# Performance work log

Hardware: AMD Instinct MI355X
Metric: run time of the kernel (lower is better)

## Reference

```python
import jax, jax.numpy as jnp
import numpy as np

PRESENCE_W = 1.0
L1_W = 1.0
B, N, M = 64, 2048, 64


def setup_inputs() -> dict:
    key = jax.random.key(0)
    k1, k2, k3, k4 = jax.random.split(key, 4)
    return {
        "predict_scores": jax.random.normal(k1, (B, N, 2), dtype=jnp.float32),
        "predict_boxes": jax.random.uniform(k2, (B, N, 4), dtype=jnp.float32),
        "scores": jax.random.randint(k3, (B, M), 0, 2, dtype=jnp.int32),
        "boxes": jax.random.uniform(k4, (B, M, 4), dtype=jnp.float32),
    }


def _cost(ps, pb, gs, gb):
    # presence[b,n,m] = -ps[b,n,gs[b,m]]
    b, n, _ = ps.shape
    m = gs.shape[1]
    idx = jnp.broadcast_to(gs[:, None, :].astype(jnp.int32), (b, n, m))
    presence = -jnp.take_along_axis(ps, idx, axis=2)            # (B,N,M)
    l1 = jnp.abs(pb[:, :, None, :] - gb[:, None, :, :]).sum(-1)  # (B,N,M)
    return PRESENCE_W * presence + L1_W * l1


def _hungarian(cost):
    # Jonker-Volgenant shortest-augmenting-path LSA (same optimum as
    # scipy.optimize.linear_sum_assignment). cost: (n, m) with n <= m.
    # Returns col4row: for each row i, the assigned column.
    n, m = cost.shape
    INF = np.inf
    u = np.zeros(n + 1)
    v = np.zeros(m + 1)
    p = np.zeros(m + 1, dtype=np.int64)   # col -> assigned row (1-based), 0=free
    way = np.zeros(m + 1, dtype=np.int64)
    for i in range(1, n + 1):
        p[0] = i
        j0 = 0
        minv = np.full(m + 1, INF)
        used = np.zeros(m + 1, dtype=bool)
        while True:
            used[j0] = True
            i0 = p[j0]
            free = ~used[1:]
            cur = cost[i0 - 1] - u[i0] - v[1:]
            mv = minv[1:]
            wy = way[1:]
            upd = free & (cur < mv)
            mv[upd] = cur[upd]
            wy[upd] = j0
            masked = np.where(free, mv, INF)
            j1 = int(np.argmin(masked)) + 1
            delta = masked[j1 - 1]
            used_idx = np.flatnonzero(used)
            u[p[used_idx]] += delta
            v[used_idx] -= delta
            mv[free] -= delta
            j0 = j1
            if p[j0] == 0:
                break
        while j0:
            j1 = way[j0]
            p[j0] = p[j1]
            j0 = j1
    col4row = np.zeros(n, dtype=np.int64)
    for j in range(1, m + 1):
        if p[j] > 0:
            col4row[p[j] - 1] = j - 1
    return col4row


def reference(predict_scores, predict_boxes, scores, boxes):
    cost = _cost(predict_scores, predict_boxes, scores, boxes)  # (B,N,M)
    c = np.asarray(jax.device_get(cost), dtype=np.float64)
    rows, cols = [], []
    for b in range(c.shape[0]):
        # transpose so the smaller side (M targets) is rows, like scipy does
        pred_for_gt = _hungarian(c[b].T)         # (M,) prediction index per target
        order = np.argsort(pred_for_gt)
        rows.append(pred_for_gt[order])          # sorted prediction indices
        cols.append(order.astype(np.int64))      # matching target indices
    row_ind = jnp.asarray(np.stack(rows), dtype=jnp.int32)  # (B,M)
    col_ind = jnp.asarray(np.stack(cols), dtype=jnp.int32)  # (B,M)
    return cost, row_ind, col_ind
```

## Files before the change

kernel.cpp:

```cpp
#include <hip/hip_runtime.h>
#include <math.h>
#include <limits.h>

#define Bb 64
#define Nn 2048
#define Mm 64

__device__ __forceinline__ float cost1(const float4 pb4, const float4 gb4,
                                       const float2 p2, const int g) {
    const float psv = (g == 0) ? p2.x : p2.y;
    float l1 = fabsf(pb4.x - gb4.x);
    l1 += fabsf(pb4.y - gb4.y);
    l1 += fabsf(pb4.z - gb4.z);
    l1 += fabsf(pb4.w - gb4.w);
    return (-psv) + l1;
}

__device__ __forceinline__ double readlane_f64_63(double x) {
    const long long v = __double_as_longlong(x);
    const int lo = __builtin_amdgcn_readlane((int)v, 63);
    const int hi = __builtin_amdgcn_readlane((int)(v >> 32), 63);
    return __longlong_as_double(((long long)hi << 32) | (unsigned int)lo);
}

__device__ __forceinline__ double readlane_f64(double x, int sl) {
    const long long v = __double_as_longlong(x);
    const int lo = __builtin_amdgcn_readlane((int)v, sl);
    const int hi = __builtin_amdgcn_readlane((int)(v >> 32), sl);
    return __longlong_as_double(((long long)hi << 32) | (unsigned int)lo);
}

__device__ __forceinline__ float readlane_f32(float x, int sl) {
    return __int_as_float(__builtin_amdgcn_readlane(__float_as_int(x), sl));
}

__device__ __forceinline__ void cost_tileA_t(
    int blk, int t, const float* __restrict__ ps, const float* __restrict__ pb,
    const int* __restrict__ gs, const float* __restrict__ gb,
    float* __restrict__ out)
{
    const int b  = blk >> 5;
    const int j0 = (blk & 31) << 6;
    const int sub = t & 15;
    const int grp = t >> 4;

    const int i4 = sub << 2;
    const int4   g4 = ((const int4*)(gs + b * Mm))[sub];
    const float4 gbq0 = ((const float4*)gb)[b * Mm + i4 + 0];
    const float4 gbq1 = ((const float4*)gb)[b * Mm + i4 + 1];
    const float4 gbq2 = ((const float4*)gb)[b * Mm + i4 + 2];
    const float4 gbq3 = ((const float4*)gb)[b * Mm + i4 + 3];
    #pragma unroll
    for (int r = 0; r < 4; ++r) {
        const int j = j0 + grp + (r << 4);
        const float2 p2  = ((const float2*)ps)[b * Nn + j];
        const float4 pb4 = ((const float4*)pb)[b * Nn + j];
        float4 o;
        o.x = cost1(pb4, gbq0, p2, g4.x);
        o.y = cost1(pb4, gbq1, p2, g4.y);
        o.z = cost1(pb4, gbq2, p2, g4.z);
        o.w = cost1(pb4, gbq3, p2, g4.w);
        ((float4*)(out + (((size_t)b * Nn + j) << 6)))[sub] = o;
    }
}

#define MIN_DPP64(VAR, CTRL)                                                    \
  {                                                                             \
    const long long mb_ = __double_as_longlong(VAR);                            \
    const int lo_ = __builtin_amdgcn_update_dpp(0, (int)mb_, CTRL, 0xf, 0xf, false);            \
    const int hi_ = __builtin_amdgcn_update_dpp(0x7ff00000, (int)(mb_ >> 32), CTRL, 0xf, 0xf, false); \
    const double om_ = __longlong_as_double(((long long)hi_ << 32) | (unsigned int)lo_);        \
    VAR = fmin(VAR, om_);                                                       \
  }

__device__ __forceinline__ void barrier_lgkm() {
    asm volatile("" ::: "memory");
    __builtin_amdgcn_s_waitcnt(0xC07F);
    __builtin_amdgcn_s_barrier();
    asm volatile("" ::: "memory");
}

struct alignas(16) Pt { double v; int ji; int pad; };

__global__ __launch_bounds__(512, 1) void hungarian_fused(
    const float* __restrict__ ps, const float* __restrict__ pb,
    const int* __restrict__ gs, const float* __restrict__ gb,
    float* __restrict__ out, float* __restrict__ out_row,
    float* __restrict__ out_col)
{
    const int bid = blockIdx.x;
    if (bid >= Bb / 2) {
        const int blk = ((bid - Bb / 2) << 1) + (threadIdx.x >> 8);
        cost_tileA_t(blk, threadIdx.x & 255, ps, pb, gs, gb, out);
        return;
    }

    __builtin_amdgcn_s_setprio(1);

    __shared__ Pt  s_part[2][2][4];
    __shared__ int s_c4r[2][Mm];
    __shared__ int s_done[2];

    const int t = threadIdx.x;
    const int lane = t & 63;
    const int wave = t >> 6;
    const int grp = wave >> 2;
    const int slot = wave & 3;
    const int tg = t & 255;
    const int b = (bid << 1) + grp;
    const double INF = __builtin_inf();

    if (t < 2) s_done[t] = 0;

    const float2* psb = (const float2*)(ps + (size_t)b * Nn * 2);
    const float4* pbb = (const float4*)(pb + (size_t)b * Nn * 4);
    float4 P[8]; float2 S[8];
    #pragma unroll
    for (int r = 0; r < 8; ++r) {
        P[r] = pbb[(tg << 3) + r];
        S[r] = psb[(tg << 3) + r];
    }
    const float4 rgb = ((const float4*)gb)[b * Mm + lane];
    const int    rg  = gs[b * Mm + lane];

    double vv[8], vreal[8];
    #pragma unroll
    for (int k = 0; k < 8; ++k) { vv[k] = 0.0; vreal[k] = 0.0; }
    double myu = 0.0;
    int mycol = 0;
    int mk = 0;
    bool inch = false;
    bool done = false;
    int i = 1, i0 = 1;
    int par = 0;

    for (;;) {
        if (!done) {
            const int sl = i0 - 1;
            float4 gb4;
            gb4.x = readlane_f32(rgb.x, sl);
            gb4.y = readlane_f32(rgb.y, sl);
            gb4.z = readlane_f32(rgb.z, sl);
            gb4.w = readlane_f32(rgb.w, sl);
            const int g = __builtin_amdgcn_readlane(rg, sl);
            const double u0 = readlane_f64(myu, sl);
            inch = inch || (lane + 1 == i0);

            double cur[8];
            #pragma unroll
            for (int k = 0; k < 8; ++k) {
                const float c = cost1(P[k], gb4, S[k], g);
                cur[k] = ((double)c - u0) - vv[k];
            }
            double v01 = cur[0]; int k01 = 0;
            if (cur[1] < v01) { v01 = cur[1]; k01 = 1; }
            double v23 = cur[2]; int k23 = 2;
            if (cur[3] < v23) { v23 = cur[3]; k23 = 3; }
            double v45 = cur[4]; int k45 = 4;
            if (cur[5] < v45) { v45 = cur[5]; k45 = 5; }
            double v67 = cur[6]; int k67 = 6;
            if (cur[7] < v67) { v67 = cur[7]; k67 = 7; }
            if (v23 < v01) { v01 = v23; k01 = k23; }
            if (v67 < v45) { v45 = v67; k45 = k67; }
            if (v45 < v01) { v01 = v45; k01 = k45; }
            const double bv = v01;
            const int bj = (tg << 3) + 1 + k01;

            double mv = bv;
            MIN_DPP64(mv, 0x111)
            MIN_DPP64(mv, 0x112)
            MIN_DPP64(mv, 0x114)
            MIN_DPP64(mv, 0x118)
            MIN_DPP64(mv, 0x142)
            MIN_DPP64(mv, 0x143)
            const double wmin = readlane_f64_63(mv);
            const unsigned long long eq = __ballot(bv == wmin);
            const int l0 = (int)__builtin_ctzll(eq);
            const int bjw = __builtin_amdgcn_readlane(bj, l0);

            const unsigned long long mw = __ballot(mycol == bjw);
            const int i0w = mw ? (int)__builtin_ctzll(mw) + 1 : 0;
            if (lane == l0) {
                Pt p; p.v = bv; p.ji = (bjw << 7) | i0w; p.pad = 0;
                s_part[par][grp][slot] = p;
            }
        }
        barrier_lgkm();
        const int dA = s_done[0];
        const int dB = s_done[1];
        if (!done) {
            const Pt pq = s_part[par][grp][lane & 3];
            double mv2 = pq.v;
            MIN_DPP64(mv2, 0xB1)
            MIN_DPP64(mv2, 0x4E)
            const unsigned long long wb = __ballot(pq.v == mv2);
            const int wsel = (int)__builtin_ctzll(wb);
            const int jiw = __builtin_amdgcn_readlane(pq.ji, wsel);
            const double delta = readlane_f64(pq.v, wsel);
            const int fjc = jiw >> 7;
            const int fi0 = jiw & 127;

            myu += inch ? delta : 0.0;
            if (mk) {
                #pragma unroll
                for (int k = 0; k < 8; ++k)
                    vreal[k] -= ((mk >> k) & 1) ? delta : 0.0;
            }

            if (fi0 == 0) {
                if (lane == i - 1) mycol = fjc;
                #pragma unroll
                for (int k = 0; k < 8; ++k) vv[k] = vreal[k];
                mk = 0; inch = false;
                ++i; i0 = i;
                if (i > Mm) {
                    done = true;
                    if (tg == 0) s_done[grp] = 1;
                }
            } else {
                i0 = fi0;
                if (((fjc - 1) >> 3) == tg) {
                    const int km = (fjc - 1) & 7;
                    #pragma unroll
                    for (int k = 0; k < 8; ++k)
                        if (k == km) vv[k] = -INF;
                    mk |= 1 << km;
                }
            }
        }
        if (dA && dB) break;
        par ^= 1;
    }

    if (wave == 0) s_c4r[0][lane] = mycol - 1;
    if (wave == 4) s_c4r[1][lane] = mycol - 1;
    __syncthreads();
    if (t < 128) {
        const int gq = t >> 6, r = t & 63;
        const int my = s_c4r[gq][r];
        int rank = 0;
        #pragma unroll 4
        for (int q = 0; q < Mm; ++q) rank += (s_c4r[gq][q] < my);
        const int bb = (bid << 1) + gq;
        out_row[bb * Mm + rank] = (float)my;
        out_col[bb * Mm + rank] = (float)r;
    }
}

extern "C" void kernel_launch(void* const* d_in, const int* in_sizes, int n_in,
                              void* d_out, int out_size, void* d_ws, size_t ws_size,
                              hipStream_t stream) {
    const float* ps = (const float*)d_in[0];
    const float* pb = (const float*)d_in[1];
    const int*   gs = (const int*)d_in[2];
    const float* gb = (const float*)d_in[3];
    float* out = (float*)d_out;
    float* out_row = out + (size_t)Bb * Nn * Mm;
    float* out_col = out_row + Bb * Mm;

    (void)d_ws; (void)ws_size;
    hungarian_fused<<<Bb / 2 + Bb * (Nn / 128), 512, 0, stream>>>(
        ps, pb, gs, gb, out, out_row, out_col);
}
```

Measured before the change: 305.3 us.

## Assign one batch per 512-thread block in Hungarian solver, 4 columns per thread

```diff
diff --git a/kernel.cpp b/kernel.cpp
--- a/kernel.cpp
+++ b/kernel.cpp
@@ -80,7 +80,7 @@
     asm volatile("" ::: "memory");
 }
 
-struct alignas(16) Pt { double v; int ji; int pad; };
+struct alignas(16) Pt { double v; int j; int pad; };
 
 __global__ __launch_bounds__(512, 1) void hungarian_fused(
     const float* __restrict__ ps, const float* __restrict__ pb,
@@ -89,161 +89,135 @@
     float* __restrict__ out_col)
 {
     const int bid = blockIdx.x;
-    if (bid >= Bb / 2) {
-        const int blk = ((bid - Bb / 2) << 1) + (threadIdx.x >> 8);
+    if (bid >= Bb) {
+        const int blk = ((bid - Bb) << 1) + (threadIdx.x >> 8);
         cost_tileA_t(blk, threadIdx.x & 255, ps, pb, gs, gb, out);
         return;
     }
 
     __builtin_amdgcn_s_setprio(1);
 
-    __shared__ Pt  s_part[2][2][4];
-    __shared__ int s_c4r[2][Mm];
-    __shared__ int s_done[2];
-
+    __shared__ Pt  s_part[2][8];
+    __shared__ int s_c4r[Mm];
+
+    const int b = bid;
     const int t = threadIdx.x;
     const int lane = t & 63;
     const int wave = t >> 6;
-    const int grp = wave >> 2;
-    const int slot = wave & 3;
-    const int tg = t & 255;
-    const int b = (bid << 1) + grp;
     const double INF = __builtin_inf();
-
-    if (t < 2) s_done[t] = 0;
 
     const float2* psb = (const float2*)(ps + (size_t)b * Nn * 2);
     const float4* pbb = (const float4*)(pb + (size_t)b * Nn * 4);
-    float4 P[8]; float2 S[8];
+    float4 P[4]; float2 S[4];
     #pragma unroll
-    for (int r = 0; r < 8; ++r) {
-        P[r] = pbb[(tg << 3) + r];
-        S[r] = psb[(tg << 3) + r];
+    for (int r = 0; r < 4; ++r) {
+        P[r] = pbb[(t << 2) + r];
+        S[r] = psb[(t << 2) + r];
     }
     const float4 rgb = ((const float4*)gb)[b * Mm + lane];
     const int    rg  = gs[b * Mm + lane];
 
-    double vv[8], vreal[8];
+    double vv[4], vreal[4];
     #pragma unroll
-    for (int k = 0; k < 8; ++k) { vv[k] = 0.0; vreal[k] = 0.0; }
+    for (int k = 0; k < 4; ++k) { vv[k] = 0.0; vreal[k] = 0.0; }
     double myu = 0.0;
     int mycol = 0;
     int mk = 0;
     bool inch = false;
-    bool done = false;
     int i = 1, i0 = 1;
     int par = 0;
 
     for (;;) {
-        if (!done) {
-            const int sl = i0 - 1;
-            float4 gb4;
-            gb4.x = readlane_f32(rgb.x, sl);
-            gb4.y = readlane_f32(rgb.y, sl);
-            gb4.z = readlane_f32(rgb.z, sl);
-            gb4.w = readlane_f32(rgb.w, sl);
-            const int g = __builtin_amdgcn_readlane(rg, sl);
-            const double u0 = readlane_f64(myu, sl);
-            inch = inch || (lane + 1 == i0);
-
-            double cur[8];
+        const int sl = i0 - 1;
+        float4 gb4;
+        gb4.x = readlane_f32(rgb.x, sl);
+        gb4.y = readlane_f32(rgb.y, sl);
+        gb4.z = readlane_f32(rgb.z, sl);
+        gb4.w = readlane_f32(rgb.w, sl);
+        const int g = __builtin_amdgcn_readlane(rg, sl);
+        const double u0 = readlane_f64(myu, sl);
+        inch = inch || (lane + 1 == i0);
+
+        double cur[4];
+        #pragma unroll
+        for (int k = 0; k < 4; ++k) {
+            const float c = cost1(P[k], gb4, S[k], g);
+            cur[k] = ((double)c - u0) - vv[k];
+        }
+        double v01 = cur[0]; int k01 = 0;
+        if (cur[1] < v01) { v01 = cur[1]; k01 = 1; }
+        double v23 = cur[2]; int k23 = 2;
+        if (cur[3] < v23) { v23 = cur[3]; k23 = 3; }
+        if (v23 < v01) { v01 = v23; k01 = k23; }
+        const double bv = v01;
+        const int bj = (t << 2) + 1 + k01;
+
+        double mv = bv;
+        MIN_DPP64(mv, 0x111)
+        MIN_DPP64(mv, 0x112)
+        MIN_DPP64(mv, 0x114)
+        MIN_DPP64(mv, 0x118)
+        MIN_DPP64(mv, 0x142)
+        MIN_DPP64(mv, 0x143)
+        const double wmin = readlane_f64_63(mv);
+        const unsigned long long eq = __ballot(bv == wmin);
+        const int l0 = (int)__builtin_ctzll(eq);
+        if (lane == l0) {
+            Pt p; p.v = bv; p.j = bj; p.pad = 0;
+            s_part[par][wave] = p;
+        }
+        barrier_lgkm();
+
+        const Pt pq = s_part[par][lane & 7];
+        double mv2 = pq.v;
+        MIN_DPP64(mv2, 0xB1)
+        MIN_DPP64(mv2, 0x4E)
+        MIN_DPP64(mv2, 0x124)
+        const unsigned long long wb = __ballot(pq.v == mv2);
+        const int wsel = (int)__builtin_ctzll(wb);
+        const int fjc = __builtin_amdgcn_readlane(pq.j, wsel);
+        const double delta = readlane_f64(pq.v, wsel);
+
+        const unsigned long long ow = __ballot(mycol == fjc);
+        const int fi0 = ow ? (int)__builtin_ctzll(ow) + 1 : 0;
+
+        myu += inch ? delta : 0.0;
+        if (mk) {
             #pragma unroll
-            for (int k = 0; k < 8; ++k) {
-                const float c = cost1(P[k], gb4, S[k], g);
-                cur[k] = ((double)c - u0) - vv[k];
+            for (int k = 0; k < 4; ++k)
+                vreal[k] -= ((mk >> k) & 1) ? delta : 0.0;
+        }
+
+        if (fi0 == 0) {
+            if (lane == i - 1) mycol = fjc;
+            #pragma unroll
+            for (int k = 0; k < 4; ++k) vv[k] = vreal[k];
+            mk = 0; inch = false;
+            ++i;
+            if (i > Mm) break;
+            i0 = i;
+        } else {
+            i0 = fi0;
+            if (((fjc - 1) >> 2) == t) {
+                const int km = (fjc - 1) & 3;
+                #pragma unroll
+                for (int k = 0; k < 4; ++k)
+                    if (k == km) vv[k] = -INF;
+                mk |= 1 << km;
             }
-            double v01 = cur[0]; int k01 = 0;
-            if (cur[1] < v01) { v01 = cur[1]; k01 = 1; }
-            double v23 = cur[2]; int k23 = 2;
-            if (cur[3] < v23) { v23 = cur[3]; k23 = 3; }
-            double v45 = cur[4]; int k45 = 4;
-            if (cur[5] < v45) { v45 = cur[5]; k45 = 5; }
-            double v67 = cur[6]; int k67 = 6;
-            if (cur[7] < v67) { v67 = cur[7]; k67 = 7; }
-            if (v23 < v01) { v01 = v23; k01 = k23; }
-            if (v67 < v45) { v45 = v67; k45 = k67; }
-            if (v45 < v01) { v01 = v45; k01 = k45; }
-            const double bv = v01;
-            const int bj = (tg << 3) + 1 + k01;
-
-            double mv = bv;
-            MIN_DPP64(mv, 0x111)
-            MIN_DPP64(mv, 0x112)
-            MIN_DPP64(mv, 0x114)
-            MIN_DPP64(mv, 0x118)
-            MIN_DPP64(mv, 0x142)
-            MIN_DPP64(mv, 0x143)
-            const double wmin = readlane_f64_63(mv);
-            const unsigned long long eq = __ballot(bv == wmin);
-            const int l0 = (int)__builtin_ctzll(eq);
-            const int bjw = __builtin_amdgcn_readlane(bj, l0);
-
-            const unsigned long long mw = __ballot(mycol == bjw);
-            const int i0w = mw ? (int)__builtin_ctzll(mw) + 1 : 0;
-            if (lane == l0) {
-                Pt p; p.v = bv; p.ji = (bjw << 7) | i0w; p.pad = 0;
-                s_part[par][grp][slot] = p;
-            }
-        }
-        barrier_lgkm();
-        const int dA = s_done[0];
-        const int dB = s_done[1];
-        if (!done) {
-            const Pt pq = s_part[par][grp][lane & 3];
-            double mv2 = pq.v;
-            MIN_DPP64(mv2, 0xB1)
-            MIN_DPP64(mv2, 0x4E)
-            const unsigned long long wb = __ballot(pq.v == mv2);
-            const int wsel = (int)__builtin_ctzll(wb);
-            const int jiw = __builtin_amdgcn_readlane(pq.ji, wsel);
-            const double delta = readlane_f64(pq.v, wsel);
-            const int fjc = jiw >> 7;
-            const int fi0 = jiw & 127;
-
-            myu += inch ? delta : 0.0;
-            if (mk) {
-                #pragma unroll
-                for (int k = 0; k < 8; ++k)
-                    vreal[k] -= ((mk >> k) & 1) ? delta : 0.0;
-            }
-
-            if (fi0 == 0) {
-                if (lane == i - 1) mycol = fjc;
-                #pragma unroll
-                for (int k = 0; k < 8; ++k) vv[k] = vreal[k];
-                mk = 0; inch = false;
-                ++i; i0 = i;
-                if (i > Mm) {
-                    done = true;
-                    if (tg == 0) s_done[grp] = 1;
-                }
-            } else {
-                i0 = fi0;
-                if (((fjc - 1) >> 3) == tg) {
-                    const int km = (fjc - 1) & 7;
-                    #pragma unroll
-                    for (int k = 0; k < 8; ++k)
-                        if (k == km) vv[k] = -INF;
-                    mk |= 1 << km;
-                }
-            }
-        }
-        if (dA && dB) break;
+        }
         par ^= 1;
     }
 
-    if (wave == 0) s_c4r[0][lane] = mycol - 1;
-    if (wave == 4) s_c4r[1][lane] = mycol - 1;
+    if (wave == 0) s_c4r[lane] = mycol - 1;
     __syncthreads();
-    if (t < 128) {
-        const int gq = t >> 6, r = t & 63;
-        const int my = s_c4r[gq][r];
+    if (t < Mm) {
+        const int my = s_c4r[t];
         int rank = 0;
         #pragma unroll 4
-        for (int q = 0; q < Mm; ++q) rank += (s_c4r[gq][q] < my);
-        const int bb = (bid << 1) + gq;
-        out_row[bb * Mm + rank] = (float)my;
-        out_col[bb * Mm + rank] = (float)r;
+        for (int q = 0; q < Mm; ++q) rank += (s_c4r[q] < my);
+        out_row[b * Mm + rank] = (float)my;
+        out_col[b * Mm + rank] = (float)t;
     }
 }
 
@@ -259,6 +233,6 @@
     float* out_col = out_row + Bb * Mm;
 
     (void)d_ws; (void)ws_size;
-    hungarian_fused<<<Bb / 2 + Bb * (Nn / 128), 512, 0, stream>>>(
+    hungarian_fused<<<Bb + Bb * (Nn / 128), 512, 0, stream>>>(
         ps, pb, gs, gb, out, out_row, out_col);
 }
```

Result: faster. 254.1 us (-16.8%).
